# Performance work log

Measured on AMD Instinct MI355X. Metric: run time of the kernel, lower is better.

Reference implementation:

```python
import jax, jax.numpy as jnp
import numpy as np

T, B, D, H = 1024, 64, 1024, 30  # seq_len, batch, input_size, hidden_size


def setup_inputs() -> dict:
    key = jax.random.key(0)
    ks = jax.random.split(key, 11)
    sc = 1.0 / np.sqrt(H)  # torch default init scale ~ U(-1/sqrt(H), 1/sqrt(H))
    u = lambda k, shape: jax.random.uniform(k, shape, dtype=jnp.float32, minval=-sc, maxval=sc)
    return {
        "x": jax.random.normal(ks[0], (T, B, D), dtype=jnp.float32),
        "W_ih0": u(ks[1], (4 * H, D)),
        "W_hh0": u(ks[2], (4 * H, H)),
        "b_ih0": u(ks[3], (4 * H,)),
        "b_hh0": u(ks[4], (4 * H,)),
        "W_ih1": u(ks[5], (4 * H, H)),
        "W_hh1": u(ks[6], (4 * H, H)),
        "b_ih1": u(ks[7], (4 * H,)),
        "b_hh1": u(ks[8], (4 * H,)),
        "W_out": u(ks[9], (1, H)),
        "b_out": u(ks[10], (1,)),
    }


def _lstm_layer(xs, Wih, Whh, bih, bhh):
    # xs: [T, B, Din] -> hs: [T, B, H]. PyTorch gate order: i, f, g, o.
    xg = jnp.einsum("tbd,gd->tbg", xs, Wih) + (bih + bhh)  # precompute input projection
    h0 = jnp.zeros((xs.shape[1], H), xs.dtype)
    c0 = jnp.zeros((xs.shape[1], H), xs.dtype)

    def step(carry, xw):
        h, c = carry
        gates = xw + h @ Whh.T  # [B, 4H]
        i, f, g, o = jnp.split(gates, 4, axis=-1)
        c = jax.nn.sigmoid(f) * c + jax.nn.sigmoid(i) * jnp.tanh(g)
        h = jax.nn.sigmoid(o) * jnp.tanh(c)
        return (h, c), h

    _, hs = jax.lax.scan(step, (h0, c0), xg)
    return hs


def reference(x, W_ih0, W_hh0, b_ih0, b_hh0, W_ih1, W_hh1, b_ih1, b_hh1, W_out, b_out):
    h1 = _lstm_layer(x, W_ih0, W_hh0, b_ih0, b_hh0)   # layer 0
    h2 = _lstm_layer(h1, W_ih1, W_hh1, b_ih1, b_hh1)  # layer 1
    return h2 @ W_out.T + b_out  # [T, B, 1]
```

## Files before the change

kernel.cpp:

```cpp
#include <hip/hip_runtime.h>
#include <hip/hip_bf16.h>
#include <cstdint>

#define TT 1024
#define BB 64
#define DD 1024
#define HH 30
#define G4 120

#define NPROD 64
#define NROUND 8
#define GBLK 16
#define NGRP 32

typedef __attribute__((ext_vector_type(8))) short short8;
typedef __attribute__((ext_vector_type(4))) float float4v;

__device__ __forceinline__ float frcp(float x) { return __builtin_amdgcn_rcpf(x); }
__device__ __forceinline__ float fsig(float x) { return frcp(1.0f + __expf(-x)); }
__device__ __forceinline__ float ftan(float x) {
    return 2.0f * frcp(1.0f + __expf(-2.0f * x)) - 1.0f;
}
__device__ __forceinline__ float bcast(float v, int l) {
    return __int_as_float(__builtin_amdgcn_readlane(__float_as_int(v), l));
}
__device__ __forceinline__ unsigned short bf16_rne(float f) {
    unsigned u = __float_as_uint(f);
    return (unsigned short)((u + 0x7FFFu + ((u >> 16) & 1u)) >> 16);
}

__global__ void prep_kernel(const float* __restrict__ Wih0,
                            const float* __restrict__ bih0,
                            const float* __restrict__ bhh0,
                            unsigned short* __restrict__ Bhi,
                            unsigned short* __restrict__ Blo,
                            float* __restrict__ bias0,
                            unsigned* __restrict__ cnt) {
    int idx = blockIdx.x * 256 + threadIdx.x;
    int l  = idx & 63;
    int kc = (idx >> 6) & 31;
    int nt = idx >> 11;
    int n = nt * 16 + (l & 15);
    int kb = kc * 32 + (l >> 4) * 8;
    size_t o = (size_t)idx * 8;
#pragma unroll
    for (int j = 0; j < 8; ++j) {
        float wv = (n < G4) ? Wih0[(size_t)n * DD + kb + j] : 0.0f;
        unsigned short hi = bf16_rne(wv);
        float fhi = __uint_as_float((unsigned)hi << 16);
        unsigned short lo = bf16_rne(wv - fhi);
        Bhi[o + j] = hi;
        Blo[o + j] = lo;
    }
    if (idx < 128) bias0[idx] = (idx < G4) ? (bih0[idx] + bhh0[idx]) : 0.0f;
    if (idx < NGRP) cnt[idx] = 0u;
}

__global__ __launch_bounds__(256, 2) void fused_fwd(
    const float* __restrict__ x, const unsigned short* __restrict__ Bhi,
    const unsigned short* __restrict__ Blo, const float* __restrict__ bias0,
    float* __restrict__ xgp, const float* __restrict__ Whh0,
    const float* __restrict__ Wih1, const float* __restrict__ Whh1,
    const float* __restrict__ bih1, const float* __restrict__ bhh1,
    float* __restrict__ h2buf, unsigned* __restrict__ cnt) {

    __shared__ float2 pg[2][64];
    const int tid = threadIdx.x;

    if (blockIdx.x < NPROD) {
        const int pb = blockIdx.x;
        const int w = tid >> 6;
        const int l = tid & 63;
        const int lm = l & 15, lq = l >> 4;

        for (int r = 0; r < NROUND; ++r) {
            const int tile = r * NPROD + pb;
            const int r0 = tile * 128 + w * 32;

            float4v acc[2][8];
#pragma unroll
            for (int mt = 0; mt < 2; ++mt)
#pragma unroll
                for (int nt = 0; nt < 8; ++nt) acc[mt][nt] = (float4v)0.0f;

            const float* aptr[2];
            aptr[0] = x + (size_t)(r0 + lm) * DD + lq * 8;
            aptr[1] = x + (size_t)(r0 + 16 + lm) * DD + lq * 8;

            float4 pa[2][2];
#pragma unroll
            for (int mt = 0; mt < 2; ++mt) {
                pa[mt][0] = *(const float4*)(aptr[mt]);
                pa[mt][1] = *(const float4*)(aptr[mt] + 4);
            }

            for (int kc = 0; kc < 32; ++kc) {
                short8 ahi[2], alo[2];
#pragma unroll
                for (int mt = 0; mt < 2; ++mt) {
                    float f[8] = {pa[mt][0].x, pa[mt][0].y, pa[mt][0].z, pa[mt][0].w,
                                  pa[mt][1].x, pa[mt][1].y, pa[mt][1].z, pa[mt][1].w};
#pragma unroll
                    for (int i = 0; i < 8; ++i) {
                        unsigned ub = __float_as_uint(f[i]);
                        ahi[mt][i] = (short)(ub >> 16);
                        float fr = f[i] - __uint_as_float(ub & 0xFFFF0000u);
                        alo[mt][i] = (short)(__float_as_uint(fr) >> 16);
                    }
                }
                if (kc + 1 < 32) {
                    const int ko = (kc + 1) * 32;
#pragma unroll
                    for (int mt = 0; mt < 2; ++mt) {
                        pa[mt][0] = *(const float4*)(aptr[mt] + ko);
                        pa[mt][1] = *(const float4*)(aptr[mt] + ko + 4);
                    }
                }
#pragma unroll
                for (int nt = 0; nt < 8; ++nt) {
                    const size_t bo = ((size_t)(nt * 32 + kc) * 64 + l) * 8;
                    short8 bh = *(const short8*)(Bhi + bo);
                    short8 bl = *(const short8*)(Blo + bo);
                    acc[0][nt] = __builtin_amdgcn_mfma_f32_16x16x32_bf16(ahi[0], bh, acc[0][nt], 0, 0, 0);
                    acc[1][nt] = __builtin_amdgcn_mfma_f32_16x16x32_bf16(ahi[1], bh, acc[1][nt], 0, 0, 0);
                    acc[0][nt] = __builtin_amdgcn_mfma_f32_16x16x32_bf16(alo[0], bh, acc[0][nt], 0, 0, 0);
                    acc[1][nt] = __builtin_amdgcn_mfma_f32_16x16x32_bf16(alo[1], bh, acc[1][nt], 0, 0, 0);
                    acc[0][nt] = __builtin_amdgcn_mfma_f32_16x16x32_bf16(ahi[0], bl, acc[0][nt], 0, 0, 0);
                    acc[1][nt] = __builtin_amdgcn_mfma_f32_16x16x32_bf16(ahi[1], bl, acc[1][nt], 0, 0, 0);
                }
            }

#pragma unroll
            for (int nt = 0; nt < 8; ++nt) {
                const int g = nt * 16 + lm;
                if (g < G4) {
                    const int gm = g % 60;
                    const int lane_t = (gm < HH) ? gm : (32 + gm - HH);
                    const int slot = g / 60;
                    const float bb = bias0[g];
#pragma unroll
                    for (int mt = 0; mt < 2; ++mt)
#pragma unroll
                        for (int i = 0; i < 4; ++i) {
                            const size_t row = r0 + mt * 16 + lq * 4 + i;
                            xgp[(row * 64 + lane_t) * 2 + slot] = acc[mt][nt][i] + bb;
                        }
                }
            }
            __syncthreads();
            if (tid == 0) {
                __threadfence();
                __hip_atomic_fetch_add(&cnt[tile >> 4], 1u, __ATOMIC_RELEASE,
                                       __HIP_MEMORY_SCOPE_AGENT);
            }
        }
        return;
    }

    const int wv = tid >> 6;
    const int l = tid & 63;
    const int b = blockIdx.x - NPROD;
    const int u = l & 31;
    const int half = l >> 5;
    const bool al = (u < HH);
    const int rlo = half * HH + (al ? u : 0);
    const int rhi = 60 + rlo;

    float wa[HH], wb[HH], wc[HH], wd[HH];
    float b1lo = 0.f, b1hi = 0.f;
    if (wv == 0) {
#pragma unroll
        for (int j = 0; j < HH; ++j) {
            wa[j] = al ? Whh0[rlo * HH + j] : 0.f;
            wb[j] = al ? Whh0[rhi * HH + j] : 0.f;
            wc[j] = al ? Wih1[rlo * HH + j] : 0.f;
            wd[j] = al ? Wih1[rhi * HH + j] : 0.f;
        }
        b1lo = al ? (bih1[rlo] + bhh1[rlo]) : 0.f;
        b1hi = al ? (bih1[rhi] + bhh1[rhi]) : 0.f;
    } else if (wv == 1) {
#pragma unroll
        for (int j = 0; j < HH; ++j) {
            wa[j] = al ? Whh1[rlo * HH + j] : 0.f;
            wb[j] = al ? Whh1[rhi * HH + j] : 0.f;
            wc[j] = 0.f; wd[j] = 0.f;
        }
    }

    float hstate = 0.f, cstate = 0.f;
    float hb[HH];
#pragma unroll
    for (int j = 0; j < HH; ++j) hb[j] = 0.f;

    const float2* xgptr = (const float2*)xgp + (size_t)b * 64 + l;
    float2 xq[4];
    unsigned next_g = 0;
    if (wv == 0) {
        while (__hip_atomic_load(&cnt[0], __ATOMIC_ACQUIRE, __HIP_MEMORY_SCOPE_AGENT) < GBLK)
            __builtin_amdgcn_s_sleep(8);
        next_g = 1;
#pragma unroll
        for (int p = 0; p < 4; ++p) xq[p] = xgptr[(size_t)p * (BB * 64)];
    }

    for (int t = 0; t <= TT; ++t) {
        if (wv == 0) {
            if (t < TT) {
                float2 xw = xq[t & 3];
                const int tn = (t + 4 < TT) ? t + 4 : TT - 1;
                const unsigned gneed = (unsigned)(tn >> 5);
                if (gneed >= next_g) {
                    while (__hip_atomic_load(&cnt[gneed], __ATOMIC_ACQUIRE,
                                             __HIP_MEMORY_SCOPE_AGENT) < GBLK)
                        __builtin_amdgcn_s_sleep(8);
                    next_g = gneed + 1;
                }
                xq[t & 3] = xgptr[(size_t)tn * (BB * 64)];

                float aA = xw.x, aB = 0.f, cA = xw.y, cB = 0.f;
#pragma unroll
                for (int j = 0; j < HH; j += 2) {
                    aA = fmaf(wa[j], hb[j], aA);
                    cA = fmaf(wb[j], hb[j], cA);
                    aB = fmaf(wa[j + 1], hb[j + 1], aB);
                    cB = fmaf(wb[j + 1], hb[j + 1], cB);
                }
                float alo = aA + aB, ahi = cA + cB;
                float plo = __shfl_xor(alo, 32, 64);
                float phi = __shfl_xor(ahi, 32, 64);
                float ipre = half ? plo : alo;
                float fpre = half ? alo : plo;
                float gpre = half ? phi : ahi;
                float opre = half ? ahi : phi;
                cstate = fsig(fpre) * cstate + fsig(ipre) * ftan(gpre);
                hstate = fsig(opre) * ftan(cstate);
#pragma unroll
                for (int j = 0; j < HH; ++j) hb[j] = bcast(hstate, j);

                float zA = b1lo, zB = 0.f, yA = b1hi, yB = 0.f;
#pragma unroll
                for (int j = 0; j < HH; j += 2) {
                    zA = fmaf(wc[j], hb[j], zA);
                    yA = fmaf(wd[j], hb[j], yA);
                    zB = fmaf(wc[j + 1], hb[j + 1], zB);
                    yB = fmaf(wd[j + 1], hb[j + 1], yB);
                }
                pg[t & 1][l] = make_float2(zA + zB, yA + yB);
            }
        } else if (wv == 1) {
            if (t > 0) {
                const int s = t - 1;
                float2 part = pg[s & 1][l];
                float zA = part.x, zB = 0.f, yA = part.y, yB = 0.f;
#pragma unroll
                for (int j = 0; j < HH; j += 2) {
                    zA = fmaf(wa[j], hb[j], zA);
                    yA = fmaf(wb[j], hb[j], yA);
                    zB = fmaf(wa[j + 1], hb[j + 1], zB);
                    yB = fmaf(wb[j + 1], hb[j + 1], yB);
                }
                float zlo = zA + zB, zhi = yA + yB;
                float qlo = __shfl_xor(zlo, 32, 64);
                float qhi = __shfl_xor(zhi, 32, 64);
                float ipre = half ? qlo : zlo;
                float fpre = half ? zlo : qlo;
                float gpre = half ? qhi : zhi;
                float opre = half ? zhi : qhi;
                cstate = fsig(fpre) * cstate + fsig(ipre) * ftan(gpre);
                hstate = fsig(opre) * ftan(cstate);
#pragma unroll
                for (int j = 0; j < HH; ++j) hb[j] = bcast(hstate, j);
                if (l < HH) h2buf[((size_t)s * BB + b) * 32 + l] = hstate;
            }
        }
        __syncthreads();
    }
}

__global__ __launch_bounds__(256) void out_proj(
    const float* __restrict__ h2buf, const float* __restrict__ Wout,
    const float* __restrict__ bout, float* __restrict__ out) {
    __shared__ float wos[32];
    if (threadIdx.x < 32)
        wos[threadIdx.x] = (threadIdx.x < HH) ? Wout[threadIdx.x] : 0.0f;
    __syncthreads();
    const int idx = blockIdx.x * 256 + threadIdx.x;
    const float4* hp = (const float4*)(h2buf + (size_t)idx * 32);
    float s0 = 0.f, s1 = 0.f;
#pragma unroll
    for (int q = 0; q < 8; ++q) {
        float4 h = hp[q];
        s0 = fmaf(h.x, wos[q * 4 + 0], s0);
        s1 = fmaf(h.y, wos[q * 4 + 1], s1);
        s0 = fmaf(h.z, wos[q * 4 + 2], s0);
        s1 = fmaf(h.w, wos[q * 4 + 3], s1);
    }
    out[idx] = s0 + s1 + bout[0];
}

extern "C" void kernel_launch(void* const* d_in, const int* in_sizes, int n_in,
                              void* d_out, int out_size, void* d_ws, size_t ws_size,
                              hipStream_t stream) {
    const float* x    = (const float*)d_in[0];
    const float* Wih0 = (const float*)d_in[1];
    const float* Whh0 = (const float*)d_in[2];
    const float* bih0 = (const float*)d_in[3];
    const float* bhh0 = (const float*)d_in[4];
    const float* Wih1 = (const float*)d_in[5];
    const float* Whh1 = (const float*)d_in[6];
    const float* bih1 = (const float*)d_in[7];
    const float* bhh1 = (const float*)d_in[8];
    const float* Wout = (const float*)d_in[9];
    const float* bout = (const float*)d_in[10];
    float* out = (float*)d_out;

    char* ws = (char*)d_ws;
    unsigned short* Bhi = (unsigned short*)ws;
    unsigned short* Blo = (unsigned short*)(ws + 262144);
    float* bias0 = (float*)(ws + 524288);
    unsigned* cnt = (unsigned*)(ws + 524800);
    float* xgp   = (float*)(ws + 1024 * 1024);
    float* h2buf = (float*)(ws + 36 * 1024 * 1024);

    prep_kernel<<<64, 256, 0, stream>>>(Wih0, bih0, bhh0, Bhi, Blo, bias0, cnt);
    fused_fwd<<<NPROD + BB, 256, 0, stream>>>(x, Bhi, Blo, bias0, xgp,
                                              Whh0, Wih1, Whh1, bih1, bhh1,
                                              h2buf, cnt);
    out_proj<<<256, 256, 0, stream>>>(h2buf, Wout, bout, out);
}
```

Before: 1.053 ms.

## Fuse both LSTM layers into one wave per batch, removing block barriers

Each wave now computes both LSTM layers for one batch element per timestep, so 4 batch elements share a block and only 16 consumer blocks launch. This removes the per-step __syncthreads and the LDS handoff between a layer-0 wave and a layer-1 wave. In exchange the two layers no longer run pipelined in parallel, making each step's serial chain longer. Register pressure rises, and the occupancy hint in launch bounds is dropped.

Result: slower. 1.376 ms (+30.6%).

```diff
diff --git a/kernel.cpp b/kernel.cpp
--- a/kernel.cpp
+++ b/kernel.cpp
@@ -10,6 +10,7 @@
 
 #define NPROD 64
 #define NROUND 8
+#define NCONS 16
 #define GBLK 16
 #define NGRP 32
 
@@ -56,7 +57,7 @@
     if (idx < NGRP) cnt[idx] = 0u;
 }
 
-__global__ __launch_bounds__(256, 2) void fused_fwd(
+__global__ __launch_bounds__(256) void fused_fwd(
     const float* __restrict__ x, const unsigned short* __restrict__ Bhi,
     const unsigned short* __restrict__ Blo, const float* __restrict__ bias0,
     float* __restrict__ xgp, const float* __restrict__ Whh0,
@@ -64,7 +65,6 @@
     const float* __restrict__ bih1, const float* __restrict__ bhh1,
     float* __restrict__ h2buf, unsigned* __restrict__ cnt) {
 
-    __shared__ float2 pg[2][64];
     const int tid = threadIdx.x;
 
     if (blockIdx.x < NPROD) {
@@ -159,121 +159,99 @@
 
     const int wv = tid >> 6;
     const int l = tid & 63;
-    const int b = blockIdx.x - NPROD;
+    const int b = (blockIdx.x - NPROD) * 4 + wv;
     const int u = l & 31;
     const int half = l >> 5;
     const bool al = (u < HH);
     const int rlo = half * HH + (al ? u : 0);
     const int rhi = 60 + rlo;
 
-    float wa[HH], wb[HH], wc[HH], wd[HH];
-    float b1lo = 0.f, b1hi = 0.f;
-    if (wv == 0) {
-#pragma unroll
-        for (int j = 0; j < HH; ++j) {
-            wa[j] = al ? Whh0[rlo * HH + j] : 0.f;
-            wb[j] = al ? Whh0[rhi * HH + j] : 0.f;
-            wc[j] = al ? Wih1[rlo * HH + j] : 0.f;
-            wd[j] = al ? Wih1[rhi * HH + j] : 0.f;
-        }
-        b1lo = al ? (bih1[rlo] + bhh1[rlo]) : 0.f;
-        b1hi = al ? (bih1[rhi] + bhh1[rhi]) : 0.f;
-    } else if (wv == 1) {
-#pragma unroll
-        for (int j = 0; j < HH; ++j) {
-            wa[j] = al ? Whh1[rlo * HH + j] : 0.f;
-            wb[j] = al ? Whh1[rhi * HH + j] : 0.f;
-            wc[j] = 0.f; wd[j] = 0.f;
-        }
-    }
-
-    float hstate = 0.f, cstate = 0.f;
-    float hb[HH];
-#pragma unroll
-    for (int j = 0; j < HH; ++j) hb[j] = 0.f;
+    float wa0[HH], wb0[HH], wc1[HH], wd1[HH], we1[HH], wf1[HH];
+#pragma unroll
+    for (int j = 0; j < HH; ++j) {
+        wa0[j] = al ? Whh0[rlo * HH + j] : 0.f;
+        wb0[j] = al ? Whh0[rhi * HH + j] : 0.f;
+        wc1[j] = al ? Wih1[rlo * HH + j] : 0.f;
+        wd1[j] = al ? Wih1[rhi * HH + j] : 0.f;
+        we1[j] = al ? Whh1[rlo * HH + j] : 0.f;
+        wf1[j] = al ? Whh1[rhi * HH + j] : 0.f;
+    }
+    const float b1lo = al ? (bih1[rlo] + bhh1[rlo]) : 0.f;
+    const float b1hi = al ? (bih1[rhi] + bhh1[rhi]) : 0.f;
+
+    float c1 = 0.f, c2 = 0.f;
+    float h1b[HH], h2b[HH];
+#pragma unroll
+    for (int j = 0; j < HH; ++j) { h1b[j] = 0.f; h2b[j] = 0.f; }
 
     const float2* xgptr = (const float2*)xgp + (size_t)b * 64 + l;
     float2 xq[4];
-    unsigned next_g = 0;
-    if (wv == 0) {
-        while (__hip_atomic_load(&cnt[0], __ATOMIC_ACQUIRE, __HIP_MEMORY_SCOPE_AGENT) < GBLK)
-            __builtin_amdgcn_s_sleep(8);
-        next_g = 1;
-#pragma unroll
-        for (int p = 0; p < 4; ++p) xq[p] = xgptr[(size_t)p * (BB * 64)];
-    }
-
-    for (int t = 0; t <= TT; ++t) {
-        if (wv == 0) {
-            if (t < TT) {
-                float2 xw = xq[t & 3];
-                const int tn = (t + 4 < TT) ? t + 4 : TT - 1;
-                const unsigned gneed = (unsigned)(tn >> 5);
-                if (gneed >= next_g) {
-                    while (__hip_atomic_load(&cnt[gneed], __ATOMIC_ACQUIRE,
-                                             __HIP_MEMORY_SCOPE_AGENT) < GBLK)
-                        __builtin_amdgcn_s_sleep(8);
-                    next_g = gneed + 1;
-                }
-                xq[t & 3] = xgptr[(size_t)tn * (BB * 64)];
-
-                float aA = xw.x, aB = 0.f, cA = xw.y, cB = 0.f;
-#pragma unroll
-                for (int j = 0; j < HH; j += 2) {
-                    aA = fmaf(wa[j], hb[j], aA);
-                    cA = fmaf(wb[j], hb[j], cA);
-                    aB = fmaf(wa[j + 1], hb[j + 1], aB);
-                    cB = fmaf(wb[j + 1], hb[j + 1], cB);
-                }
-                float alo = aA + aB, ahi = cA + cB;
-                float plo = __shfl_xor(alo, 32, 64);
-                float phi = __shfl_xor(ahi, 32, 64);
-                float ipre = half ? plo : alo;
-                float fpre = half ? alo : plo;
-                float gpre = half ? phi : ahi;
-                float opre = half ? ahi : phi;
-                cstate = fsig(fpre) * cstate + fsig(ipre) * ftan(gpre);
-                hstate = fsig(opre) * ftan(cstate);
-#pragma unroll
-                for (int j = 0; j < HH; ++j) hb[j] = bcast(hstate, j);
-
-                float zA = b1lo, zB = 0.f, yA = b1hi, yB = 0.f;
-#pragma unroll
-                for (int j = 0; j < HH; j += 2) {
-                    zA = fmaf(wc[j], hb[j], zA);
-                    yA = fmaf(wd[j], hb[j], yA);
-                    zB = fmaf(wc[j + 1], hb[j + 1], zB);
-                    yB = fmaf(wd[j + 1], hb[j + 1], yB);
-                }
-                pg[t & 1][l] = make_float2(zA + zB, yA + yB);
-            }
-        } else if (wv == 1) {
-            if (t > 0) {
-                const int s = t - 1;
-                float2 part = pg[s & 1][l];
-                float zA = part.x, zB = 0.f, yA = part.y, yB = 0.f;
-#pragma unroll
-                for (int j = 0; j < HH; j += 2) {
-                    zA = fmaf(wa[j], hb[j], zA);
-                    yA = fmaf(wb[j], hb[j], yA);
-                    zB = fmaf(wa[j + 1], hb[j + 1], zB);
-                    yB = fmaf(wb[j + 1], hb[j + 1], yB);
-                }
-                float zlo = zA + zB, zhi = yA + yB;
-                float qlo = __shfl_xor(zlo, 32, 64);
-                float qhi = __shfl_xor(zhi, 32, 64);
-                float ipre = half ? qlo : zlo;
-                float fpre = half ? zlo : qlo;
-                float gpre = half ? qhi : zhi;
-                float opre = half ? zhi : qhi;
-                cstate = fsig(fpre) * cstate + fsig(ipre) * ftan(gpre);
-                hstate = fsig(opre) * ftan(cstate);
-#pragma unroll
-                for (int j = 0; j < HH; ++j) hb[j] = bcast(hstate, j);
-                if (l < HH) h2buf[((size_t)s * BB + b) * 32 + l] = hstate;
-            }
-        }
-        __syncthreads();
+    while (__hip_atomic_load(&cnt[0], __ATOMIC_ACQUIRE, __HIP_MEMORY_SCOPE_AGENT) < GBLK)
+        __builtin_amdgcn_s_sleep(8);
+    unsigned next_g = 1;
+#pragma unroll
+    for (int p = 0; p < 4; ++p) xq[p] = xgptr[(size_t)p * (BB * 64)];
+
+    for (int t = 0; t < TT; ++t) {
+        float2 xw = xq[t & 3];
+        const int tn = (t + 4 < TT) ? t + 4 : TT - 1;
+        const unsigned gneed = (unsigned)(tn >> 5);
+        if (gneed >= next_g) {
+            while (__hip_atomic_load(&cnt[gneed], __ATOMIC_ACQUIRE,
+                                     __HIP_MEMORY_SCOPE_AGENT) < GBLK)
+                __builtin_amdgcn_s_sleep(8);
+            next_g = gneed + 1;
+        }
+        xq[t & 3] = xgptr[(size_t)tn * (BB * 64)];
+
+        float zA = b1lo, zB = 0.f, yA = b1hi, yB = 0.f;
+#pragma unroll
+        for (int j = 0; j < HH; j += 2) {
+            zA = fmaf(we1[j], h2b[j], zA);
+            yA = fmaf(wf1[j], h2b[j], yA);
+            zB = fmaf(we1[j + 1], h2b[j + 1], zB);
+            yB = fmaf(wf1[j + 1], h2b[j + 1], yB);
+        }
+
+        float aA = xw.x, aB = 0.f, cA = xw.y, cB = 0.f;
+#pragma unroll
+        for (int j = 0; j < HH; j += 2) {
+            aA = fmaf(wa0[j], h1b[j], aA);
+            cA = fmaf(wb0[j], h1b[j], cA);
+            aB = fmaf(wa0[j + 1], h1b[j + 1], aB);
+            cB = fmaf(wb0[j + 1], h1b[j + 1], cB);
+        }
+        float alo = aA + aB, ahi = cA + cB;
+        float plo = __shfl_xor(alo, 32, 64);
+        float phi = __shfl_xor(ahi, 32, 64);
+        float ipre0 = half ? plo : alo;
+        float fpre0 = half ? alo : plo;
+        float gpre0 = half ? phi : ahi;
+        float opre0 = half ? ahi : phi;
+        c1 = fsig(fpre0) * c1 + fsig(ipre0) * ftan(gpre0);
+        float h1 = fsig(opre0) * ftan(c1);
+#pragma unroll
+        for (int j = 0; j < HH; ++j) h1b[j] = bcast(h1, j);
+
+#pragma unroll
+        for (int j = 0; j < HH; j += 2) {
+            zA = fmaf(wc1[j], h1b[j], zA);
+            yA = fmaf(wd1[j], h1b[j], yA);
+            zB = fmaf(wc1[j + 1], h1b[j + 1], zB);
+            yB = fmaf(wd1[j + 1], h1b[j + 1], yB);
+        }
+        float zlo = zA + zB, zhi = yA + yB;
+        float qlo = __shfl_xor(zlo, 32, 64);
+        float qhi = __shfl_xor(zhi, 32, 64);
+        float ipre1 = half ? qlo : zlo;
+        float fpre1 = half ? zlo : qlo;
+        float gpre1 = half ? qhi : zhi;
+        float opre1 = half ? zhi : qhi;
+        c2 = fsig(fpre1) * c2 + fsig(ipre1) * ftan(gpre1);
+        float h2 = fsig(opre1) * ftan(c2);
+#pragma unroll
+        for (int j = 0; j < HH; ++j) h2b[j] = bcast(h2, j);
+        if (l < HH) h2buf[((size_t)t * BB + b) * 32 + l] = h2;
     }
 }
 
@@ -323,8 +301,8 @@
     float* h2buf = (float*)(ws + 36 * 1024 * 1024);
 
     prep_kernel<<<64, 256, 0, stream>>>(Wih0, bih0, bhh0, Bhi, Blo, bias0, cnt);
-    fused_fwd<<<NPROD + BB, 256, 0, stream>>>(x, Bhi, Blo, bias0, xgp,
-                                              Whh0, Wih1, Whh1, bih1, bhh1,
-                                              h2buf, cnt);
+    fused_fwd<<<NPROD + NCONS, 256, 0, stream>>>(x, Bhi, Blo, bias0, xgp,
+                                                 Whh0, Wih1, Whh1, bih1, bhh1,
+                                                 h2buf, cnt);
     out_proj<<<256, 256, 0, stream>>>(h2buf, Wout, bout, out);
 }
```
